# Kernel optimization log

Hardware: AMD Instinct MI355X
Metric: run time of the kernel (lower is better)

Reference implementation:

```python
import jax, jax.numpy as jnp
import numpy as np

WS = (8, 8, 8)        # window size
SS = (4, 4, 4)        # shift size
HEADS = 4
DIM = 128
N = WS[0] * WS[1] * WS[2]  # 512 tokens per window


def _relative_position_index():
    # identical math to ShiftedWindowAttention.define_relative_position_index
    coords = np.stack(np.meshgrid(np.arange(WS[0]), np.arange(WS[1]), np.arange(WS[2]), indexing='ij'))
    cf = coords.reshape(3, -1)                       # [3, N]
    rel = (cf[:, :, None] - cf[:, None, :]).transpose(1, 2, 0).copy()  # [N, N, 3]
    rel[..., 0] += WS[0] - 1
    rel[..., 1] += WS[1] - 1
    rel[..., 2] += WS[2] - 1
    rel[..., 0] *= (2 * WS[2] - 1) * (2 * WS[1] - 1)
    rel[..., 1] *= 2 * WS[2] - 1
    return rel.sum(-1).reshape(-1).astype(np.int32)  # [N*N]


def _shift_attn_mask(H, W, D):
    # static shift mask, same as the torch slice-loop construction
    m = np.zeros((H, W, D), dtype=np.float32)
    hs = ((0, -WS[0]), (-WS[0], -SS[0]), (-SS[0], None))
    ws = ((0, -WS[1]), (-WS[1], -SS[1]), (-SS[1], None))
    ds = ((0, -WS[2]), (-WS[2], -SS[2]), (-SS[2], None))
    cnt = 0
    for h in hs:
        for w in ws:
            for d in ds:
                m[h[0]:h[1], w[0]:w[1], d[0]:d[1]] = cnt
                cnt += 1
    nH, nW, nD = H // WS[0], W // WS[1], D // WS[2]
    m = m.reshape(nH, WS[0], nW, WS[1], nD, WS[2]).transpose(0, 2, 4, 1, 3, 5).reshape(nH * nW * nD, N)
    diff = m[:, None, :] - m[:, :, None]
    return np.where(diff != 0, np.float32(-100.0), np.float32(0.0))  # [nWin, N, N]


def setup_inputs() -> dict:
    key = jax.random.key(0)
    ks = jax.random.split(key, 6)
    x = jax.random.normal(ks[0], (1, 32, 32, 32, DIM), dtype=jnp.float32)
    qkv_weight = jax.random.normal(ks[1], (3 * DIM, DIM), dtype=jnp.float32) * 0.02
    qkv_bias = jax.random.normal(ks[2], (3 * DIM,), dtype=jnp.float32) * 0.02
    proj_weight = jax.random.normal(ks[3], (DIM, DIM), dtype=jnp.float32) * 0.02
    proj_bias = jax.random.normal(ks[4], (DIM,), dtype=jnp.float32) * 0.02
    tbl = (2 * WS[0] - 1) * (2 * WS[1] - 1) * (2 * WS[2] - 1)
    rpb_table = jax.random.normal(ks[5], (tbl, HEADS), dtype=jnp.float32) * 0.02
    rp_index = jnp.asarray(_relative_position_index())
    return {"x": x, "qkv_weight": qkv_weight, "qkv_bias": qkv_bias,
            "proj_weight": proj_weight, "proj_bias": proj_bias,
            "rpb_table": rpb_table, "rp_index": rp_index}


def reference(x, qkv_weight, qkv_bias, proj_weight, proj_bias, rpb_table, rp_index):
    B, H, W, D, C = x.shape
    hd = C // HEADS
    # relative position bias: [1, heads, N, N]
    bias = rpb_table[rp_index].reshape(N, N, HEADS).transpose(2, 0, 1)[None]
    # cyclic shift (H,W,D divisible by window -> no padding branch)
    xs = jnp.roll(x, shift=(-SS[0], -SS[1], -SS[2]), axis=(1, 2, 3))
    nH, nW, nD = H // WS[0], W // WS[1], D // WS[2]
    nWin = nH * nW * nD
    # window partition -> [B*nWin, N, C]
    xw = xs.reshape(B, nH, WS[0], nW, WS[1], nD, WS[2], C)
    xw = xw.transpose(0, 1, 3, 5, 2, 4, 6, 7).reshape(B * nWin, N, C)
    qkv = xw @ qkv_weight.T + qkv_bias
    qkv = qkv.reshape(B * nWin, N, 3, HEADS, hd).transpose(2, 0, 3, 1, 4)
    q, k, v = qkv[0], qkv[1], qkv[2]          # each [B*nWin, heads, N, hd]
    q = q * jnp.float32(hd ** -0.5)
    attn = jnp.einsum('whnd,whmd->whnm', q, k) + bias
    mask = jnp.asarray(_shift_attn_mask(H, W, D))  # [nWin, N, N] static
    attn = attn.reshape(B, nWin, HEADS, N, N) + mask[None, :, None]
    attn = jax.nn.softmax(attn.reshape(B * nWin, HEADS, N, N), axis=-1)
    out = jnp.einsum('whnm,whmd->wnhd', attn, v).reshape(B * nWin, N, C)
    out = out @ proj_weight.T + proj_bias
    # reverse window partition
    out = out.reshape(B, nH, nW, nD, WS[0], WS[1], WS[2], C)
    out = out.transpose(0, 1, 4, 2, 5, 3, 6, 7).reshape(B, H, W, D, C)
    return jnp.roll(out, shift=(SS[0], SS[1], SS[2]), axis=(1, 2, 3))
```

## Files before the change

kernel.cpp:

```cpp
#include <hip/hip_runtime.h>
#include <hip/hip_bf16.h>
#include <math.h>


#define NTOT 262144

typedef float     f32x16 __attribute__((ext_vector_type(16)));
typedef __bf16    bf16x8 __attribute__((ext_vector_type(8)));
typedef _Float16  f16x8  __attribute__((ext_vector_type(8)));
typedef _Float16  f16x4  __attribute__((ext_vector_type(4)));
typedef unsigned int u32x4 __attribute__((ext_vector_type(4)));

__device__ __forceinline__ unsigned int pkbf16(float a, float b) {
  __hip_bfloat16 x = __float2bfloat16(a), y = __float2bfloat16(b);
  return (unsigned int)__builtin_bit_cast(unsigned short, x) |
         ((unsigned int)__builtin_bit_cast(unsigned short, y) << 16);
}

__global__ void k_bias(const float* __restrict__ rpb, const int* __restrict__ rpi,
                       float* __restrict__ bias_full,
                       const float* __restrict__ qkvw, const float* __restrict__ projw,
                       _Float16* __restrict__ wq, _Float16* __restrict__ wp) {
  int idx = blockIdx.x * 256 + threadIdx.x;
  int t = rpi[idx];
  float4 b4 = *reinterpret_cast<const float4*>(rpb + 4 * t);
  bias_full[0 * NTOT + idx] = b4.x;
  bias_full[1 * NTOT + idx] = b4.y;
  bias_full[2 * NTOT + idx] = b4.z;
  bias_full[3 * NTOT + idx] = b4.w;
  if (idx < 65536) {
    if (idx < 49152) wq[idx] = (_Float16)qkvw[idx];
    else             wp[idx - 49152] = (_Float16)projw[idx - 49152];
  }
}

__global__ __launch_bounds__(256, 2) void k_qkv(
    const float* __restrict__ x, const _Float16* __restrict__ wq,
    const float* __restrict__ qkvb,
    __hip_bfloat16* __restrict__ qb, __hip_bfloat16* __restrict__ kb,
    __hip_bfloat16* __restrict__ vb) {
  __shared__ unsigned short As[128 * 128];
  __shared__ unsigned short Bs[128 * 128];
  const int tid = threadIdx.x;
  const int bm = blockIdx.x;
  const int nc = bm >> 8;
  const int mt = bm & 255;
  const int win = mt >> 2, t128 = mt & 3;
  const int wh = win >> 4, ww = (win >> 2) & 3, wd = win & 3;

#pragma unroll
  for (int u = 0; u < 8; ++u) {
    int f = u * 256 + tid;
    int row = f >> 4, seg = f & 15;
    int n = t128 * 128 + row;
    int lh = n >> 6, lw = (n >> 3) & 7, ld = n & 7;
    int sh = (wh * 8 + lh + 4) & 31;
    int sw = (ww * 8 + lw + 4) & 31;
    int sd = (wd * 8 + ld + 4) & 31;
    const float* src = x + ((sh * 32 + sw) * 32 + sd) * 128 + seg * 8;
    float4 a0 = *(const float4*)src;
    float4 a1 = *(const float4*)(src + 4);
    f16x8 hv;
    hv[0] = (_Float16)a0.x; hv[1] = (_Float16)a0.y;
    hv[2] = (_Float16)a0.z; hv[3] = (_Float16)a0.w;
    hv[4] = (_Float16)a1.x; hv[5] = (_Float16)a1.y;
    hv[6] = (_Float16)a1.z; hv[7] = (_Float16)a1.w;
    int slot = seg ^ (row & 15);
    *(u32x4*)(&As[row * 128 + slot * 8]) = __builtin_bit_cast(u32x4, hv);
  }
#pragma unroll
  for (int u = 0; u < 8; ++u) {
    int f = u * 256 + tid;
    int row = f >> 4, seg = f & 15;
    u32x4 wv = *(const u32x4*)(wq + (nc * 128 + row) * 128 + seg * 8);
    int slot = seg ^ (row & 15);
    *(u32x4*)(&Bs[row * 128 + slot * 8]) = wv;
  }
  __syncthreads();

  const int wave = tid >> 6, lane = tid & 63;
  const int lq = lane & 31, h = lane >> 5;
  const int wm = wave >> 1, wn = wave & 1;

  f32x16 a00, a01, a10, a11;
#pragma unroll
  for (int r = 0; r < 16; ++r) { a00[r] = 0.f; a01[r] = 0.f; a10[r] = 0.f; a11[r] = 0.f; }

#pragma unroll
  for (int ks = 0; ks < 8; ++ks) {
    int r0 = wm * 64 + lq, r1 = wm * 64 + 32 + lq;
    int c0 = wn * 64 + lq, c1 = wn * 64 + 32 + lq;
    int sl = ks * 2 + h;
    f16x8 af0 = __builtin_bit_cast(f16x8, *(const u32x4*)(&As[r0 * 128 + (sl ^ (r0 & 15)) * 8]));
    f16x8 af1 = __builtin_bit_cast(f16x8, *(const u32x4*)(&As[r1 * 128 + (sl ^ (r1 & 15)) * 8]));
    f16x8 bf0 = __builtin_bit_cast(f16x8, *(const u32x4*)(&Bs[c0 * 128 + (sl ^ (c0 & 15)) * 8]));
    f16x8 bf1 = __builtin_bit_cast(f16x8, *(const u32x4*)(&Bs[c1 * 128 + (sl ^ (c1 & 15)) * 8]));
    a00 = __builtin_amdgcn_mfma_f32_32x32x16_f16(af0, bf0, a00, 0, 0, 0);
    a01 = __builtin_amdgcn_mfma_f32_32x32x16_f16(af0, bf1, a01, 0, 0, 0);
    a10 = __builtin_amdgcn_mfma_f32_32x32x16_f16(af1, bf0, a10, 0, 0, 0);
    a11 = __builtin_amdgcn_mfma_f32_32x32x16_f16(af1, bf1, a11, 0, 0, 0);
  }

  const float scale = 0.17677669529663687f;
  float bias0 = qkvb[nc * 128 + wn * 64 + lq];
  float bias1 = qkvb[nc * 128 + wn * 64 + 32 + lq];

#define EPI_QK(ACC, MI, NI, DST, DO_SCALE)                                    \
  {                                                                           \
    int head = wn * 2 + (NI);                                                 \
    size_t whb = (size_t)(win * 4 + head);                                    \
    float bc = (NI) ? bias1 : bias0;                                          \
    _Pragma("unroll")                                                         \
    for (int r = 0; r < 16; ++r) {                                            \
      int row32 = (r & 3) + 8 * (r >> 2) + 4 * h;                             \
      int n = t128 * 128 + wm * 64 + (MI) * 32 + row32;                       \
      float val = ACC[r] + bc;                                                \
      if (DO_SCALE) val *= scale;                                             \
      DST[(whb * 512 + n) * 32 + lq] = __float2bfloat16(val);                 \
    }                                                                         \
  }
#define EPI_V(ACC, MI, NI)                                                    \
  {                                                                           \
    int head = wn * 2 + (NI);                                                 \
    size_t whb = (size_t)(win * 4 + head);                                    \
    float bc = (NI) ? bias1 : bias0;                                          \
    _Pragma("unroll")                                                         \
    for (int g = 0; g < 4; ++g) {                                             \
      int n0 = t128 * 128 + wm * 64 + (MI) * 32 + g * 8 + 4 * h;              \
      uint2 u = make_uint2(pkbf16(ACC[g * 4 + 0] + bc, ACC[g * 4 + 1] + bc),  \
                           pkbf16(ACC[g * 4 + 2] + bc, ACC[g * 4 + 3] + bc)); \
      *(uint2*)(vb + (whb * 32 + lq) * 512 + n0) = u;                         \
    }                                                                         \
  }

  if (nc == 0) {
    EPI_QK(a00, 0, 0, qb, 1); EPI_QK(a01, 0, 1, qb, 1);
    EPI_QK(a10, 1, 0, qb, 1); EPI_QK(a11, 1, 1, qb, 1);
  } else if (nc == 1) {
    EPI_QK(a00, 0, 0, kb, 0); EPI_QK(a01, 0, 1, kb, 0);
    EPI_QK(a10, 1, 0, kb, 0); EPI_QK(a11, 1, 1, kb, 0);
  } else {
    EPI_V(a00, 0, 0); EPI_V(a01, 0, 1);
    EPI_V(a10, 1, 0); EPI_V(a11, 1, 1);
  }
}

__global__ __launch_bounds__(256) void k_attn(
    const __hip_bfloat16* __restrict__ qb, const __hip_bfloat16* __restrict__ kb,
    const __hip_bfloat16* __restrict__ vb, const float* __restrict__ bias_full,
    _Float16* __restrict__ ao) {
  __shared__ unsigned short Ks[64 * 40];
  __shared__ unsigned short Vs[32 * 72];
  __shared__ unsigned char regid[512];

  const int tid = threadIdx.x;
  const int b = blockIdx.x;
  const int win = b >> 4, head = (b >> 2) & 3, qblk = b & 3;
  const int wh = win >> 4, ww = (win >> 2) & 3, wd = win & 3;
  const int wave = tid >> 6, lane = tid & 63;
  const int lq = lane & 31, h = lane >> 5;
  const int q = qblk * 128 + wave * 32 + lq;

#pragma unroll
  for (int i = 0; i < 2; ++i) {
    int n = tid + i * 256;
    int lh = n >> 6, lw = (n >> 3) & 7, ld = n & 7;
    regid[n] = (unsigned char)(((wh == 3) ? (lh < 4 ? 1 : 2) : 0) * 9 +
                               ((ww == 3) ? (lw < 4 ? 1 : 2) : 0) * 3 +
                               ((wd == 3) ? (ld < 4 ? 1 : 2) : 0));
  }
  const int qlh = q >> 6, qlw = (q >> 3) & 7, qld = q & 7;
  const unsigned int rn =
      (unsigned)(((wh == 3) ? (qlh < 4 ? 1 : 2) : 0) * 9 +
                 ((ww == 3) ? (qlw < 4 ? 1 : 2) : 0) * 3 +
                 ((wd == 3) ? (qld < 4 ? 1 : 2) : 0));

  const size_t whb = (size_t)(win * 4 + head);
  const __hip_bfloat16* qrow = qb + (whb * 512 + q) * 32;
  bf16x8 qf0 = __builtin_bit_cast(bf16x8, *(const u32x4*)(qrow + h * 8));
  bf16x8 qf1 = __builtin_bit_cast(bf16x8, *(const u32x4*)(qrow + 16 + h * 8));

  const __hip_bfloat16* kg = kb + whb * 512 * 32;
  const __hip_bfloat16* vg = vb + whb * 32 * 512;
  const float* brow = bias_full + ((size_t)head * 512 + q) * 512;

  float m_run = -3.0e38f, l_run = 0.f;
  f32x16 o;
#pragma unroll
  for (int r = 0; r < 16; ++r) o[r] = 0.f;

  for (int chk = 0; chk < 8; ++chk) {
    __syncthreads();
    {
      int row = tid >> 2, seg = tid & 3;
      *(u32x4*)(&Ks[row * 40 + seg * 8]) =
          *(const u32x4*)(kg + (chk * 64 + row) * 32 + seg * 8);
      int d = tid >> 3, seg2 = tid & 7;
      *(u32x4*)(&Vs[d * 72 + seg2 * 8]) =
          *(const u32x4*)(vg + d * 512 + chk * 64 + seg2 * 8);
    }
    __syncthreads();

#pragma unroll
    for (int sub = 0; sub < 2; ++sub) {
      const int kbase = chk * 64 + sub * 32;

      bf16x8 kf0 = __builtin_bit_cast(bf16x8,
          *(const u32x4*)(&Ks[(sub * 32 + lq) * 40 + h * 8]));
      bf16x8 kf1 = __builtin_bit_cast(bf16x8,
          *(const u32x4*)(&Ks[(sub * 32 + lq) * 40 + 16 + h * 8]));
      f32x16 c;
#pragma unroll
      for (int r = 0; r < 16; ++r) c[r] = 0.f;
      c = __builtin_amdgcn_mfma_f32_32x32x16_bf16(kf0, qf0, c, 0, 0, 0);
      c = __builtin_amdgcn_mfma_f32_32x32x16_bf16(kf1, qf1, c, 0, 0, 0);

      float bias_s[16];
      unsigned int rm4[4];
#pragma unroll
      for (int j = 0; j < 4; ++j) {
        float4 b4 = *(const float4*)(brow + kbase + h * 4 + j * 8);
        bias_s[j * 4 + 0] = b4.x; bias_s[j * 4 + 1] = b4.y;
        bias_s[j * 4 + 2] = b4.z; bias_s[j * 4 + 3] = b4.w;
        rm4[j] = *(const unsigned int*)(&regid[kbase + h * 4 + j * 8]);
      }

      float s[16];
#pragma unroll
      for (int r = 0; r < 16; ++r) {
        int j = r >> 2, i = r & 3;
        float mval = (((rm4[j] >> (8 * i)) & 255u) == rn) ? 0.f : -100.f;
        s[r] = c[r] + bias_s[r] + mval;
      }

      float tmax = s[0];
#pragma unroll
      for (int r = 1; r < 16; ++r) tmax = fmaxf(tmax, s[r]);
      tmax = fmaxf(tmax, __shfl_xor(tmax, 32, 64));
      float m_new = fmaxf(m_run, tmax);
      float alpha = __expf(m_run - m_new);
      float p[16], lsum = 0.f;
#pragma unroll
      for (int r = 0; r < 16; ++r) { p[r] = __expf(s[r] - m_new); lsum += p[r]; }
      lsum += __shfl_xor(lsum, 32, 64);
      l_run = l_run * alpha + lsum;
      m_run = m_new;
#pragma unroll
      for (int r = 0; r < 16; ++r) o[r] *= alpha;

      unsigned int bw[8];
#pragma unroll
      for (int g = 0; g < 8; ++g) bw[g] = pkbf16(p[2 * g], p[2 * g + 1]);

#pragma unroll
      for (int kc = 0; kc < 2; ++kc) {
        unsigned int b0 = bw[kc * 4 + 0], b1 = bw[kc * 4 + 1];
        unsigned int b2 = bw[kc * 4 + 2], b3 = bw[kc * 4 + 3];
        unsigned int sb0 = __shfl_xor(b0, 32, 64), sb1 = __shfl_xor(b1, 32, 64);
        unsigned int sb2 = __shfl_xor(b2, 32, 64), sb3 = __shfl_xor(b3, 32, 64);
        u32x4 pw;
        pw.x = h ? sb2 : b0;
        pw.y = h ? sb3 : b1;
        pw.z = h ? b2 : sb0;
        pw.w = h ? b3 : sb1;
        bf16x8 pf = __builtin_bit_cast(bf16x8, pw);
        bf16x8 vf = __builtin_bit_cast(bf16x8,
            *(const u32x4*)(&Vs[lq * 72 + sub * 32 + kc * 16 + h * 8]));
        o = __builtin_amdgcn_mfma_f32_32x32x16_bf16(vf, pf, o, 0, 0, 0);
      }
    }
  }

  const float inv = 1.f / l_run;
  _Float16* orow = ao + ((size_t)(win * 512 + q)) * 128 + head * 32;
#pragma unroll
  for (int j = 0; j < 4; ++j) {
    int d0 = j * 8 + h * 4;
    f16x4 t;
    t[0] = (_Float16)(o[j * 4 + 0] * inv);
    t[1] = (_Float16)(o[j * 4 + 1] * inv);
    t[2] = (_Float16)(o[j * 4 + 2] * inv);
    t[3] = (_Float16)(o[j * 4 + 3] * inv);
    *(f16x4*)(orow + d0) = t;
  }
}

__global__ __launch_bounds__(256, 2) void k_proj(
    const _Float16* __restrict__ ao, const _Float16* __restrict__ wp,
    const float* __restrict__ pb, float* __restrict__ out) {
  __shared__ unsigned short As[128 * 128];
  __shared__ unsigned short Bs[128 * 128];
  const int tid = threadIdx.x;
  const int mt = blockIdx.x;
  const int win = mt >> 2, t128 = mt & 3;
  const int wh = win >> 4, ww = (win >> 2) & 3, wd = win & 3;

#pragma unroll
  for (int u = 0; u < 8; ++u) {
    int f = u * 256 + tid;
    int row = f >> 4, seg = f & 15;
    u32x4 av = *(const u32x4*)(ao + ((size_t)(win * 512 + t128 * 128 + row)) * 128 + seg * 8);
    int slot = seg ^ (row & 15);
    *(u32x4*)(&As[row * 128 + slot * 8]) = av;
  }
#pragma unroll
  for (int u = 0; u < 8; ++u) {
    int f = u * 256 + tid;
    int row = f >> 4, seg = f & 15;
    u32x4 wv = *(const u32x4*)(wp + row * 128 + seg * 8);
    int slot = seg ^ (row & 15);
    *(u32x4*)(&Bs[row * 128 + slot * 8]) = wv;
  }
  __syncthreads();

  const int wave = tid >> 6, lane = tid & 63;
  const int lq = lane & 31, h = lane >> 5;
  const int wm = wave >> 1, wn = wave & 1;

  f32x16 a00, a01, a10, a11;
#pragma unroll
  for (int r = 0; r < 16; ++r) { a00[r] = 0.f; a01[r] = 0.f; a10[r] = 0.f; a11[r] = 0.f; }

#pragma unroll
  for (int ks = 0; ks < 8; ++ks) {
    int r0 = wm * 64 + lq, r1 = wm * 64 + 32 + lq;
    int c0 = wn * 64 + lq, c1 = wn * 64 + 32 + lq;
    int sl = ks * 2 + h;
    f16x8 af0 = __builtin_bit_cast(f16x8, *(const u32x4*)(&As[r0 * 128 + (sl ^ (r0 & 15)) * 8]));
    f16x8 af1 = __builtin_bit_cast(f16x8, *(const u32x4*)(&As[r1 * 128 + (sl ^ (r1 & 15)) * 8]));
    f16x8 bf0 = __builtin_bit_cast(f16x8, *(const u32x4*)(&Bs[c0 * 128 + (sl ^ (c0 & 15)) * 8]));
    f16x8 bf1 = __builtin_bit_cast(f16x8, *(const u32x4*)(&Bs[c1 * 128 + (sl ^ (c1 & 15)) * 8]));
    a00 = __builtin_amdgcn_mfma_f32_32x32x16_f16(af0, bf0, a00, 0, 0, 0);
    a01 = __builtin_amdgcn_mfma_f32_32x32x16_f16(af0, bf1, a01, 0, 0, 0);
    a10 = __builtin_amdgcn_mfma_f32_32x32x16_f16(af1, bf0, a10, 0, 0, 0);
    a11 = __builtin_amdgcn_mfma_f32_32x32x16_f16(af1, bf1, a11, 0, 0, 0);
  }

  float bias0 = pb[wn * 64 + lq];
  float bias1 = pb[wn * 64 + 32 + lq];

#define EPI_P(ACC, MI, NI)                                                    \
  {                                                                           \
    int col = wn * 64 + (NI) * 32 + lq;                                       \
    float bc = (NI) ? bias1 : bias0;                                          \
    _Pragma("unroll")                                                         \
    for (int r = 0; r < 16; ++r) {                                            \
      int row32 = (r & 3) + 8 * (r >> 2) + 4 * h;                             \
      int n = t128 * 128 + wm * 64 + (MI) * 32 + row32;                       \
      int lh = n >> 6, lw = (n >> 3) & 7, ld = n & 7;                         \
      int dh = (wh * 8 + lh + 4) & 31;                                        \
      int dw = (ww * 8 + lw + 4) & 31;                                        \
      int dd = (wd * 8 + ld + 4) & 31;                                        \
      out[(size_t)((dh * 32 + dw) * 32 + dd) * 128 + col] = ACC[r] + bc;      \
    }                                                                         \
  }
  EPI_P(a00, 0, 0); EPI_P(a01, 0, 1); EPI_P(a10, 1, 0); EPI_P(a11, 1, 1);
}

extern "C" void kernel_launch(void* const* d_in, const int* in_sizes, int n_in,
                              void* d_out, int out_size, void* d_ws, size_t ws_size,
                              hipStream_t stream) {
  const float* x    = (const float*)d_in[0];
  const float* qkvw = (const float*)d_in[1];
  const float* qkvb = (const float*)d_in[2];
  const float* pw   = (const float*)d_in[3];
  const float* pb   = (const float*)d_in[4];
  const float* rpb  = (const float*)d_in[5];
  const int*   rpi  = (const int*)d_in[6];
  float* out = (float*)d_out;

  char* base = (char*)d_ws;
  __hip_bfloat16* qbuf = (__hip_bfloat16*)(base);
  __hip_bfloat16* kbuf = (__hip_bfloat16*)(base + 8388608);
  __hip_bfloat16* vbuf = (__hip_bfloat16*)(base + 16777216);
  _Float16* ao = (_Float16*)(base + 25165824);
  float* bf = (float*)(base + 33554432);
  _Float16* wq = (_Float16*)(base + 37748736);
  _Float16* wp = (_Float16*)(base + 37847040);

  hipLaunchKernelGGL(k_bias, dim3(1024), dim3(256), 0, stream, rpb, rpi, bf, qkvw, pw, wq, wp);
  hipLaunchKernelGGL(k_qkv,  dim3(768),  dim3(256), 0, stream, x, wq, qkvb, qbuf, kbuf, vbuf);
  hipLaunchKernelGGL(k_attn, dim3(1024), dim3(256), 0, stream, qbuf, kbuf, vbuf, bf, ao);
  hipLaunchKernelGGL(k_proj, dim3(256),  dim3(256), 0, stream, ao, wp, pb, out);
}
```

Before: 153.4 us.

## Restructure window attention: 64 queries per wave, bf16 log2 bias, double-buffered K/V

```diff
diff --git a/kernel.cpp b/kernel.cpp
--- a/kernel.cpp
+++ b/kernel.cpp
@@ -16,18 +16,22 @@
   return (unsigned int)__builtin_bit_cast(unsigned short, x) |
          ((unsigned int)__builtin_bit_cast(unsigned short, y) << 16);
 }
+__device__ __forceinline__ unsigned short bfbits(float v) {
+  return __builtin_bit_cast(unsigned short, __float2bfloat16(v));
+}
 
 __global__ void k_bias(const float* __restrict__ rpb, const int* __restrict__ rpi,
-                       float* __restrict__ bias_full,
+                       unsigned short* __restrict__ biasb,
                        const float* __restrict__ qkvw, const float* __restrict__ projw,
                        _Float16* __restrict__ wq, _Float16* __restrict__ wp) {
   int idx = blockIdx.x * 256 + threadIdx.x;
   int t = rpi[idx];
   float4 b4 = *reinterpret_cast<const float4*>(rpb + 4 * t);
-  bias_full[0 * NTOT + idx] = b4.x;
-  bias_full[1 * NTOT + idx] = b4.y;
-  bias_full[2 * NTOT + idx] = b4.z;
-  bias_full[3 * NTOT + idx] = b4.w;
+  const float L2E = 1.4426950408889634f;
+  biasb[0 * NTOT + idx] = bfbits(b4.x * L2E);
+  biasb[1 * NTOT + idx] = bfbits(b4.y * L2E);
+  biasb[2 * NTOT + idx] = bfbits(b4.z * L2E);
+  biasb[3 * NTOT + idx] = bfbits(b4.w * L2E);
   if (idx < 65536) {
     if (idx < 49152) wq[idx] = (_Float16)qkvw[idx];
     else             wp[idx - 49152] = (_Float16)projw[idx - 49152];
@@ -101,7 +105,7 @@
     a11 = __builtin_amdgcn_mfma_f32_32x32x16_f16(af1, bf1, a11, 0, 0, 0);
   }
 
-  const float scale = 0.17677669529663687f;
+  const float scale = (float)(0.17677669529663687 * 1.4426950408889634);
   float bias0 = qkvb[nc * 128 + wn * 64 + lq];
   float bias1 = qkvb[nc * 128 + wn * 64 + 32 + lq];
 
@@ -147,141 +151,180 @@
 
 __global__ __launch_bounds__(256) void k_attn(
     const __hip_bfloat16* __restrict__ qb, const __hip_bfloat16* __restrict__ kb,
-    const __hip_bfloat16* __restrict__ vb, const float* __restrict__ bias_full,
+    const __hip_bfloat16* __restrict__ vb, const unsigned short* __restrict__ biasb,
     _Float16* __restrict__ ao) {
-  __shared__ unsigned short Ks[64 * 40];
-  __shared__ unsigned short Vs[32 * 72];
+  __shared__ unsigned short Ks[2][64 * 40];
+  __shared__ unsigned short Vs[2][32 * 72];
   __shared__ unsigned char regid[512];
 
   const int tid = threadIdx.x;
   const int b = blockIdx.x;
-  const int win = b >> 4, head = (b >> 2) & 3, qblk = b & 3;
+  const int win = b >> 3, head = (b >> 1) & 3, half = b & 1;
   const int wh = win >> 4, ww = (win >> 2) & 3, wd = win & 3;
   const int wave = tid >> 6, lane = tid & 63;
   const int lq = lane & 31, h = lane >> 5;
-  const int q = qblk * 128 + wave * 32 + lq;
-
-#pragma unroll
-  for (int i = 0; i < 2; ++i) {
-    int n = tid + i * 256;
-    int lh = n >> 6, lw = (n >> 3) & 7, ld = n & 7;
-    regid[n] = (unsigned char)(((wh == 3) ? (lh < 4 ? 1 : 2) : 0) * 9 +
-                               ((ww == 3) ? (lw < 4 ? 1 : 2) : 0) * 3 +
-                               ((wd == 3) ? (ld < 4 ? 1 : 2) : 0));
-  }
-  const int qlh = q >> 6, qlw = (q >> 3) & 7, qld = q & 7;
-  const unsigned int rn =
-      (unsigned)(((wh == 3) ? (qlh < 4 ? 1 : 2) : 0) * 9 +
-                 ((ww == 3) ? (qlw < 4 ? 1 : 2) : 0) * 3 +
-                 ((wd == 3) ? (qld < 4 ? 1 : 2) : 0));
+  const int qA = half * 256 + wave * 64 + lq;
+  const int qB = qA + 32;
+  const bool has_mask = (wh == 3) || (ww == 3) || (wd == 3);
+
+  unsigned rnA = 0, rnB = 0;
+  if (has_mask) {
+#pragma unroll
+    for (int i = 0; i < 2; ++i) {
+      int n = tid + i * 256;
+      int lh = n >> 6, lw = (n >> 3) & 7, ld = n & 7;
+      regid[n] = (unsigned char)(((wh == 3) ? (lh < 4 ? 1 : 2) : 0) * 9 +
+                                 ((ww == 3) ? (lw < 4 ? 1 : 2) : 0) * 3 +
+                                 ((wd == 3) ? (ld < 4 ? 1 : 2) : 0));
+    }
+    {
+      int n = qA;
+      int lh = n >> 6, lw = (n >> 3) & 7, ld = n & 7;
+      rnA = (unsigned)(((wh == 3) ? (lh < 4 ? 1 : 2) : 0) * 9 +
+                       ((ww == 3) ? (lw < 4 ? 1 : 2) : 0) * 3 +
+                       ((wd == 3) ? (ld < 4 ? 1 : 2) : 0));
+      n = qB; lh = n >> 6; lw = (n >> 3) & 7; ld = n & 7;
+      rnB = (unsigned)(((wh == 3) ? (lh < 4 ? 1 : 2) : 0) * 9 +
+                       ((ww == 3) ? (lw < 4 ? 1 : 2) : 0) * 3 +
+                       ((wd == 3) ? (ld < 4 ? 1 : 2) : 0));
+    }
+  }
 
   const size_t whb = (size_t)(win * 4 + head);
-  const __hip_bfloat16* qrow = qb + (whb * 512 + q) * 32;
-  bf16x8 qf0 = __builtin_bit_cast(bf16x8, *(const u32x4*)(qrow + h * 8));
-  bf16x8 qf1 = __builtin_bit_cast(bf16x8, *(const u32x4*)(qrow + 16 + h * 8));
+  const __hip_bfloat16* qrowA = qb + (whb * 512 + qA) * 32;
+  const __hip_bfloat16* qrowB = qb + (whb * 512 + qB) * 32;
+  bf16x8 qfA0 = __builtin_bit_cast(bf16x8, *(const u32x4*)(qrowA + h * 8));
+  bf16x8 qfA1 = __builtin_bit_cast(bf16x8, *(const u32x4*)(qrowA + 16 + h * 8));
+  bf16x8 qfB0 = __builtin_bit_cast(bf16x8, *(const u32x4*)(qrowB + h * 8));
+  bf16x8 qfB1 = __builtin_bit_cast(bf16x8, *(const u32x4*)(qrowB + 16 + h * 8));
 
   const __hip_bfloat16* kg = kb + whb * 512 * 32;
   const __hip_bfloat16* vg = vb + whb * 32 * 512;
-  const float* brow = bias_full + ((size_t)head * 512 + q) * 512;
-
-  float m_run = -3.0e38f, l_run = 0.f;
-  f32x16 o;
-#pragma unroll
-  for (int r = 0; r < 16; ++r) o[r] = 0.f;
+  const unsigned short* browA = biasb + ((size_t)head * 512 + qA) * 512;
+  const unsigned short* browB = biasb + ((size_t)head * 512 + qB) * 512;
+
+  float mA = -3.0e38f, lA = 0.f, mB = -3.0e38f, lB = 0.f;
+  f32x16 oA, oB;
+#pragma unroll
+  for (int r = 0; r < 16; ++r) { oA[r] = 0.f; oB[r] = 0.f; }
+
+  const int srow = tid >> 2, sseg = tid & 3;
+  const int svd = tid >> 3, sseg2 = tid & 7;
+  u32x4 kreg, vreg;
+#define GLOAD(CHK)                                                            \
+  { kreg = *(const u32x4*)(kg + ((CHK) * 64 + srow) * 32 + sseg * 8);         \
+    vreg = *(const u32x4*)(vg + svd * 512 + (CHK) * 64 + sseg2 * 8); }
+#define LWRITE(BUF)                                                           \
+  { *(u32x4*)(&Ks[BUF][srow * 40 + sseg * 8]) = kreg;                         \
+    *(u32x4*)(&Vs[BUF][svd * 72 + sseg2 * 8]) = vreg; }
+
+  GLOAD(0); LWRITE(0);
+  __syncthreads();
+
+  auto stream_step = [&](f32x16 c, float& m_run, float& l_run, f32x16& o,
+                         const unsigned short* brow, unsigned rn,
+                         bf16x8 vf0, bf16x8 vf1, int kbase) {
+    float s[16];
+#pragma unroll
+    for (int j = 0; j < 4; ++j) {
+      uint2 bb = *(const uint2*)(brow + kbase + h * 4 + j * 8);
+      float b0 = __uint_as_float(bb.x << 16);
+      float b1 = __uint_as_float(bb.x & 0xFFFF0000u);
+      float b2 = __uint_as_float(bb.y << 16);
+      float b3 = __uint_as_float(bb.y & 0xFFFF0000u);
+      if (has_mask) {
+        unsigned rm = *(const unsigned*)(&regid[kbase + h * 4 + j * 8]);
+        b0 += ((rm & 255u) == rn) ? 0.f : -144.2695041f;
+        b1 += (((rm >> 8) & 255u) == rn) ? 0.f : -144.2695041f;
+        b2 += (((rm >> 16) & 255u) == rn) ? 0.f : -144.2695041f;
+        b3 += (((rm >> 24)) == rn) ? 0.f : -144.2695041f;
+      }
+      s[j * 4 + 0] = c[j * 4 + 0] + b0;
+      s[j * 4 + 1] = c[j * 4 + 1] + b1;
+      s[j * 4 + 2] = c[j * 4 + 2] + b2;
+      s[j * 4 + 3] = c[j * 4 + 3] + b3;
+    }
+    float x0 = fmaxf(s[0], s[8]),  x1 = fmaxf(s[1], s[9]);
+    float x2 = fmaxf(s[2], s[10]), x3 = fmaxf(s[3], s[11]);
+    float x4 = fmaxf(s[4], s[12]), x5 = fmaxf(s[5], s[13]);
+    float x6 = fmaxf(s[6], s[14]), x7 = fmaxf(s[7], s[15]);
+    x0 = fmaxf(x0, x4); x1 = fmaxf(x1, x5); x2 = fmaxf(x2, x6); x3 = fmaxf(x3, x7);
+    x0 = fmaxf(x0, x2); x1 = fmaxf(x1, x3);
+    float tmax = fmaxf(x0, x1);
+    tmax = fmaxf(tmax, __shfl_xor(tmax, 32, 64));
+    if (!__all(tmax <= m_run + 11.5415603f)) {
+      float mn = fmaxf(m_run, tmax);
+      float alpha = exp2f(m_run - mn);
+      l_run *= alpha;
+#pragma unroll
+      for (int r = 0; r < 16; ++r) o[r] *= alpha;
+      m_run = mn;
+    }
+    float p[16], lsum = 0.f;
+#pragma unroll
+    for (int r = 0; r < 16; ++r) { p[r] = exp2f(s[r] - m_run); lsum += p[r]; }
+    lsum += __shfl_xor(lsum, 32, 64);
+    l_run += lsum;
+    unsigned bw[8];
+#pragma unroll
+    for (int g = 0; g < 8; ++g) bw[g] = pkbf16(p[2 * g], p[2 * g + 1]);
+#pragma unroll
+    for (int kc = 0; kc < 2; ++kc) {
+      unsigned b0 = bw[kc * 4 + 0], b1 = bw[kc * 4 + 1];
+      unsigned b2 = bw[kc * 4 + 2], b3 = bw[kc * 4 + 3];
+      unsigned sb0 = __shfl_xor(b0, 32, 64), sb1 = __shfl_xor(b1, 32, 64);
+      unsigned sb2 = __shfl_xor(b2, 32, 64), sb3 = __shfl_xor(b3, 32, 64);
+      u32x4 pw;
+      pw.x = h ? sb2 : b0;
+      pw.y = h ? sb3 : b1;
+      pw.z = h ? b2 : sb0;
+      pw.w = h ? b3 : sb1;
+      bf16x8 pf = __builtin_bit_cast(bf16x8, pw);
+      o = __builtin_amdgcn_mfma_f32_32x32x16_bf16(kc ? vf1 : vf0, pf, o, 0, 0, 0);
+    }
+  };
 
   for (int chk = 0; chk < 8; ++chk) {
-    __syncthreads();
-    {
-      int row = tid >> 2, seg = tid & 3;
-      *(u32x4*)(&Ks[row * 40 + seg * 8]) =
-          *(const u32x4*)(kg + (chk * 64 + row) * 32 + seg * 8);
-      int d = tid >> 3, seg2 = tid & 7;
-      *(u32x4*)(&Vs[d * 72 + seg2 * 8]) =
-          *(const u32x4*)(vg + d * 512 + chk * 64 + seg2 * 8);
-    }
-    __syncthreads();
+    const int cur = chk & 1;
+    if (chk < 7) GLOAD(chk + 1);
 
 #pragma unroll
     for (int sub = 0; sub < 2; ++sub) {
       const int kbase = chk * 64 + sub * 32;
-
-      bf16x8 kf0 = __builtin_bit_cast(bf16x8,
-          *(const u32x4*)(&Ks[(sub * 32 + lq) * 40 + h * 8]));
-      bf16x8 kf1 = __builtin_bit_cast(bf16x8,
-          *(const u32x4*)(&Ks[(sub * 32 + lq) * 40 + 16 + h * 8]));
-      f32x16 c;
-#pragma unroll
-      for (int r = 0; r < 16; ++r) c[r] = 0.f;
-      c = __builtin_amdgcn_mfma_f32_32x32x16_bf16(kf0, qf0, c, 0, 0, 0);
-      c = __builtin_amdgcn_mfma_f32_32x32x16_bf16(kf1, qf1, c, 0, 0, 0);
-
-      float bias_s[16];
-      unsigned int rm4[4];
-#pragma unroll
-      for (int j = 0; j < 4; ++j) {
-        float4 b4 = *(const float4*)(brow + kbase + h * 4 + j * 8);
-        bias_s[j * 4 + 0] = b4.x; bias_s[j * 4 + 1] = b4.y;
-        bias_s[j * 4 + 2] = b4.z; bias_s[j * 4 + 3] = b4.w;
-        rm4[j] = *(const unsigned int*)(&regid[kbase + h * 4 + j * 8]);
-      }
-
-      float s[16];
-#pragma unroll
-      for (int r = 0; r < 16; ++r) {
-        int j = r >> 2, i = r & 3;
-        float mval = (((rm4[j] >> (8 * i)) & 255u) == rn) ? 0.f : -100.f;
-        s[r] = c[r] + bias_s[r] + mval;
-      }
-
-      float tmax = s[0];
-#pragma unroll
-      for (int r = 1; r < 16; ++r) tmax = fmaxf(tmax, s[r]);
-      tmax = fmaxf(tmax, __shfl_xor(tmax, 32, 64));
-      float m_new = fmaxf(m_run, tmax);
-      float alpha = __expf(m_run - m_new);
-      float p[16], lsum = 0.f;
-#pragma unroll
-      for (int r = 0; r < 16; ++r) { p[r] = __expf(s[r] - m_new); lsum += p[r]; }
-      lsum += __shfl_xor(lsum, 32, 64);
-      l_run = l_run * alpha + lsum;
-      m_run = m_new;
-#pragma unroll
-      for (int r = 0; r < 16; ++r) o[r] *= alpha;
-
-      unsigned int bw[8];
-#pragma unroll
-      for (int g = 0; g < 8; ++g) bw[g] = pkbf16(p[2 * g], p[2 * g + 1]);
-
-#pragma unroll
-      for (int kc = 0; kc < 2; ++kc) {
-        unsigned int b0 = bw[kc * 4 + 0], b1 = bw[kc * 4 + 1];
-        unsigned int b2 = bw[kc * 4 + 2], b3 = bw[kc * 4 + 3];
-        unsigned int sb0 = __shfl_xor(b0, 32, 64), sb1 = __shfl_xor(b1, 32, 64);
-        unsigned int sb2 = __shfl_xor(b2, 32, 64), sb3 = __shfl_xor(b3, 32, 64);
-        u32x4 pw;
-        pw.x = h ? sb2 : b0;
-        pw.y = h ? sb3 : b1;
-        pw.z = h ? b2 : sb0;
-        pw.w = h ? b3 : sb1;
-        bf16x8 pf = __builtin_bit_cast(bf16x8, pw);
-        bf16x8 vf = __builtin_bit_cast(bf16x8,
-            *(const u32x4*)(&Vs[lq * 72 + sub * 32 + kc * 16 + h * 8]));
-        o = __builtin_amdgcn_mfma_f32_32x32x16_bf16(vf, pf, o, 0, 0, 0);
-      }
-    }
-  }
-
-  const float inv = 1.f / l_run;
-  _Float16* orow = ao + ((size_t)(win * 512 + q)) * 128 + head * 32;
+      const unsigned short* KsC = Ks[cur];
+      const unsigned short* VsC = Vs[cur];
+      bf16x8 kf0 = __builtin_bit_cast(bf16x8, *(const u32x4*)(&KsC[(sub * 32 + lq) * 40 + h * 8]));
+      bf16x8 kf1 = __builtin_bit_cast(bf16x8, *(const u32x4*)(&KsC[(sub * 32 + lq) * 40 + 16 + h * 8]));
+      f32x16 cA, cB;
+#pragma unroll
+      for (int r = 0; r < 16; ++r) { cA[r] = 0.f; cB[r] = 0.f; }
+      cA = __builtin_amdgcn_mfma_f32_32x32x16_bf16(kf0, qfA0, cA, 0, 0, 0);
+      cA = __builtin_amdgcn_mfma_f32_32x32x16_bf16(kf1, qfA1, cA, 0, 0, 0);
+      cB = __builtin_amdgcn_mfma_f32_32x32x16_bf16(kf0, qfB0, cB, 0, 0, 0);
+      cB = __builtin_amdgcn_mfma_f32_32x32x16_bf16(kf1, qfB1, cB, 0, 0, 0);
+      bf16x8 vf0 = __builtin_bit_cast(bf16x8, *(const u32x4*)(&VsC[lq * 72 + sub * 32 + h * 8]));
+      bf16x8 vf1 = __builtin_bit_cast(bf16x8, *(const u32x4*)(&VsC[lq * 72 + sub * 32 + 16 + h * 8]));
+      stream_step(cA, mA, lA, oA, browA, rnA, vf0, vf1, kbase);
+      stream_step(cB, mB, lB, oB, browB, rnB, vf0, vf1, kbase);
+    }
+
+    if (chk < 7) LWRITE(cur ^ 1);
+    __syncthreads();
+  }
+
+  const float invA = 1.f / lA, invB = 1.f / lB;
+  _Float16* orowA = ao + ((size_t)(win * 512 + qA)) * 128 + head * 32;
+  _Float16* orowB = ao + ((size_t)(win * 512 + qB)) * 128 + head * 32;
 #pragma unroll
   for (int j = 0; j < 4; ++j) {
     int d0 = j * 8 + h * 4;
-    f16x4 t;
-    t[0] = (_Float16)(o[j * 4 + 0] * inv);
-    t[1] = (_Float16)(o[j * 4 + 1] * inv);
-    t[2] = (_Float16)(o[j * 4 + 2] * inv);
-    t[3] = (_Float16)(o[j * 4 + 3] * inv);
-    *(f16x4*)(orow + d0) = t;
+    f16x4 tA, tB;
+    tA[0] = (_Float16)(oA[j * 4 + 0] * invA); tA[1] = (_Float16)(oA[j * 4 + 1] * invA);
+    tA[2] = (_Float16)(oA[j * 4 + 2] * invA); tA[3] = (_Float16)(oA[j * 4 + 3] * invA);
+    tB[0] = (_Float16)(oB[j * 4 + 0] * invB); tB[1] = (_Float16)(oB[j * 4 + 1] * invB);
+    tB[2] = (_Float16)(oB[j * 4 + 2] * invB); tB[3] = (_Float16)(oB[j * 4 + 3] * invB);
+    *(f16x4*)(orowA + d0) = tA;
+    *(f16x4*)(orowB + d0) = tB;
   }
 }
 
@@ -374,12 +417,12 @@
   __hip_bfloat16* kbuf = (__hip_bfloat16*)(base + 8388608);
   __hip_bfloat16* vbuf = (__hip_bfloat16*)(base + 16777216);
   _Float16* ao = (_Float16*)(base + 25165824);
-  float* bf = (float*)(base + 33554432);
-  _Float16* wq = (_Float16*)(base + 37748736);
-  _Float16* wp = (_Float16*)(base + 37847040);
-
-  hipLaunchKernelGGL(k_bias, dim3(1024), dim3(256), 0, stream, rpb, rpi, bf, qkvw, pw, wq, wp);
+  unsigned short* biasb = (unsigned short*)(base + 33554432);
+  _Float16* wq = (_Float16*)(base + 35651584);
+  _Float16* wp = (_Float16*)(base + 35749888);
+
+  hipLaunchKernelGGL(k_bias, dim3(1024), dim3(256), 0, stream, rpb, rpi, biasb, qkvw, pw, wq, wp);
   hipLaunchKernelGGL(k_qkv,  dim3(768),  dim3(256), 0, stream, x, wq, qkvb, qbuf, kbuf, vbuf);
-  hipLaunchKernelGGL(k_attn, dim3(1024), dim3(256), 0, stream, qbuf, kbuf, vbuf, bf, ao);
+  hipLaunchKernelGGL(k_attn, dim3(512),  dim3(256), 0, stream, qbuf, kbuf, vbuf, biasb, ao);
   hipLaunchKernelGGL(k_proj, dim3(256),  dim3(256), 0, stream, ao, wp, pb, out);
 }
```

Result: slower. 158.5 us (+3.3%).
